# Kernel tuning notes

Measured on AMD Instinct MI355X. Metric: run time of the kernel, lower is better.

## Reference

```python
import jax, jax.numpy as jnp
import numpy as np

N, E, D, G, OUT = 100000, 1600000, 64, 2048, 16
BN_EPS = 1e-5


def setup_inputs() -> dict:
    key = jax.random.key(0)
    ks = jax.random.split(key, 24)
    s = 1.0 / np.sqrt(D)
    inp = {
        "x": jax.random.normal(ks[0], (N, D), jnp.float32),
        "edge_index": jax.random.randint(ks[1], (2, E), 0, N, jnp.int64),
        "batch": jnp.sort(jax.random.randint(ks[2], (N,), 0, G, jnp.int64)),
        # layer 0: custom_mp (mean-aggregated linear message)
        "W0": jax.random.normal(ks[3], (D, D), jnp.float32) * s,
        "b0": jnp.zeros((D,), jnp.float32),
        # layer 1: SAGE (lin_l on mean-agg neighbors + lin_r on root, lin_r bias-free)
        "Wl": jax.random.normal(ks[4], (D, D), jnp.float32) * s,
        "bl": jnp.zeros((D,), jnp.float32),
        "Wr": jax.random.normal(ks[5], (D, D), jnp.float32) * s,
        # layer 2: GIN (mlp((1+eps)*x + sum-agg), eps=0)
        "W2a": jax.random.normal(ks[6], (D, D), jnp.float32) * s,
        "b2a": jnp.zeros((D,), jnp.float32),
        "W2b": jax.random.normal(ks[7], (D, D), jnp.float32) * s,
        "b2b": jnp.zeros((D,), jnp.float32),
        # layer 3: GraphConv (lin_rel on sum-agg + bias, lin_root bias-free)
        "Wrel": jax.random.normal(ks[8], (D, D), jnp.float32) * s,
        "brel": jnp.zeros((D,), jnp.float32),
        "Wroot": jax.random.normal(ks[9], (D, D), jnp.float32) * s,
        # BatchNorm affine params per layer [4, D]
        "gammas": jnp.ones((4, D), jnp.float32),
        "betas": jnp.zeros((4, D), jnp.float32),
        # output head
        "Wout": jax.random.normal(ks[10], (D, OUT), jnp.float32) * s,
        "bout": jnp.zeros((OUT,), jnp.float32),
    }
    return inp


def _seg_sum(msgs, idx, n):
    return jax.ops.segment_sum(msgs, idx, num_segments=n)


def _mean_agg(h, src, dst, n):
    # mean of incoming messages; isolated nodes get 0 (PyG mean semantics)
    s = _seg_sum(h[src], dst, n)
    cnt = _seg_sum(jnp.ones((src.shape[0], 1), h.dtype), dst, n)
    return s / jnp.maximum(cnt, 1.0), (cnt > 0).astype(h.dtype)


def _bn_elu(h, gamma, beta):
    # training-mode BatchNorm1d (biased var) + ELU; dropout is eval-mode no-op
    mu = jnp.mean(h, axis=0)
    var = jnp.mean(jnp.square(h - mu), axis=0)
    h = (h - mu) * jax.lax.rsqrt(var + BN_EPS) * gamma + beta
    return jax.nn.elu(h)


def reference(x, edge_index, batch, W0, b0, Wl, bl, Wr, W2a, b2a, W2b, b2b,
              Wrel, brel, Wroot, gammas, betas, Wout, bout):
    src, dst = edge_index[0], edge_index[1]
    n = x.shape[0]

    # layer 0: custom_mp -> mean_j lin(x_j); lin then mean == mean then lin,
    # except bias must vanish on isolated nodes (mean of zero messages is 0).
    agg, mask = _mean_agg(x, src, dst, n)
    h = agg @ W0 + b0 * mask
    h = _bn_elu(h, gammas[0], betas[0])

    # layer 1: SAGEConv
    agg, _ = _mean_agg(h, src, dst, n)
    h = agg @ Wl + bl + h @ Wr
    h = _bn_elu(h, gammas[1], betas[1])

    # layer 2: GINConv, eps = 0
    s = _seg_sum(h[src], dst, n)
    z = (h + s) @ W2a + b2a
    h = jax.nn.relu(z) @ W2b + b2b
    h = _bn_elu(h, gammas[2], betas[2])

    # layer 3: GraphConv (sum aggregation)
    s = _seg_sum(h[src], dst, n)
    h = s @ Wrel + brel + h @ Wroot
    h = _bn_elu(h, gammas[3], betas[3])

    # global mean pool over graphs, then linear head
    ps = _seg_sum(h, batch, G)
    pc = _seg_sum(jnp.ones((n, 1), h.dtype), batch, G)
    pooled = ps / jnp.maximum(pc, 1.0)
    return pooled @ Wout + bout
```

## Files before the change

kernel.cpp:

```cpp
#include <hip/hip_runtime.h>
#include <math.h>

#define D 64
#define NB_SCAN 256

typedef unsigned short ushort_t;
typedef __attribute__((ext_vector_type(8))) short bf16x8;
typedef __attribute__((ext_vector_type(4))) float f32x4;

__device__ __forceinline__ ushort_t f2bf(float f) {
  unsigned int u = __float_as_uint(f);
  unsigned int r = (u + 0x7fffu + ((u >> 16) & 1u)) >> 16;
  return (ushort_t)r;
}

__device__ __forceinline__ float bf2f(ushort_t b) {
  return __uint_as_float((unsigned int)b << 16);
}

__global__ void hist_kernel(const int* __restrict__ dst, int* __restrict__ hist, int E) {
  int i = blockIdx.x * blockDim.x + threadIdx.x;
  int stride = gridDim.x * blockDim.x;
  for (int e = i; e < E; e += stride) {
    int d = __builtin_nontemporal_load(dst + e);
    atomicAdd(&hist[d], 1);
  }
}

__global__ void scanA_kernel(const int* __restrict__ hist, int* __restrict__ blocksum, int N) {
  __shared__ int red[256];
  int b = blockIdx.x, t = threadIdx.x;
  int chunk = (N + NB_SCAN - 1) / NB_SCAN;
  int beg = b * chunk;
  int end = min(beg + chunk, N);
  int s = 0;
  for (int i = beg + t; i < end; i += 256) s += hist[i];
  red[t] = s;
  __syncthreads();
  for (int off = 128; off > 0; off >>= 1) {
    if (t < off) red[t] += red[t + off];
    __syncthreads();
  }
  if (t == 0) blocksum[b] = red[0];
}

__global__ void scanB_kernel(const int* __restrict__ blocksum, int* __restrict__ blockoff,
                             int* __restrict__ rowptr_last) {
  __shared__ int sm[NB_SCAN];
  int t = threadIdx.x;
  sm[t] = blocksum[t];
  __syncthreads();
  for (int off = 1; off < NB_SCAN; off <<= 1) {
    int v = (t >= off) ? sm[t - off] : 0;
    __syncthreads();
    sm[t] += v;
    __syncthreads();
  }
  blockoff[t] = (t == 0) ? 0 : sm[t - 1];
  if (t == NB_SCAN - 1) rowptr_last[0] = sm[t];
}

__global__ void scanC_kernel(const int* __restrict__ hist, const int* __restrict__ blockoff,
                             int* __restrict__ rowptr, float* __restrict__ degf, int N) {
  __shared__ int sm[256];
  int b = blockIdx.x, t = threadIdx.x;
  int chunk = (N + NB_SCAN - 1) / NB_SCAN;
  int beg = b * chunk;
  int end = min(beg + chunk, N);
  int sub = (chunk + 255) / 256;
  int mybeg = beg + t * sub;
  int myend = min(mybeg + sub, end);
  int s = 0;
  for (int i = mybeg; i < myend; ++i) s += hist[i];
  sm[t] = s;
  __syncthreads();
  for (int off = 1; off < 256; off <<= 1) {
    int v = (t >= off) ? sm[t - off] : 0;
    __syncthreads();
    sm[t] += v;
    __syncthreads();
  }
  int run = blockoff[b] + ((t == 0) ? 0 : sm[t - 1]);
  for (int i = mybeg; i < myend; ++i) {
    int h = hist[i];
    rowptr[i] = run;
    degf[i] = (float)h;
    run += h;
  }
}

__global__ void fillp_kernel(const int* __restrict__ src, const int* __restrict__ dst,
                             const int* __restrict__ rowptr, int* __restrict__ cursor,
                             int* __restrict__ csr_src, int E, int N) {
  int r = blockIdx.x & 7;
  int c = blockIdx.x >> 3;
  int nchunk = gridDim.x >> 3;
  int lo = (r * N) >> 3;
  int hi = ((r + 1) * N) >> 3;
  int per = (E + nchunk - 1) / nchunk;
  int beg = c * per;
  int end = min(beg + per, E);
  for (int e = beg + (int)threadIdx.x; e < end; e += (int)blockDim.x) {
    int d = __builtin_nontemporal_load(dst + e);
    if (d >= lo && d < hi) {
      int s = __builtin_nontemporal_load(src + e);
      int pos = atomicAdd(&cursor[d], 1);
      csr_src[rowptr[d] + pos] = s;
    }
  }
}

__global__ void cvt_kernel(const float* __restrict__ in, ushort_t* __restrict__ outb, int total4) {
  int i = blockIdx.x * blockDim.x + threadIdx.x;
  int stride = gridDim.x * blockDim.x;
  const float4* in4 = (const float4*)in;
  for (int idx = i; idx < total4; idx += stride) {
    float4 v = in4[idx];
    ushort4 u;
    u.x = f2bf(v.x); u.y = f2bf(v.y); u.z = f2bf(v.z); u.w = f2bf(v.w);
    ((ushort4*)outb)[idx] = u;
  }
}

__global__ void packw_kernel(const float* __restrict__ W, ushort_t* __restrict__ Wp) {
  int idx = blockIdx.x * blockDim.x + threadIdx.x;
  if (idx >= 4096) return;
  int i = idx & 7;
  int lane = (idx >> 3) & 63;
  int ct = (idx >> 9) & 3;
  int kt = idx >> 11;
  int k = kt * 32 + ((lane >> 4) << 3) + i;
  int c = (ct << 4) + (lane & 15);
  Wp[idx] = f2bf(W[k * D + c]);
}

__global__ void gatherb_kernel(const ushort_t* __restrict__ hb, const int* __restrict__ rowptr,
                               const int* __restrict__ csr_src, ushort_t* __restrict__ aggb, int N) {
  int lane = threadIdx.x & 63;
  int wid = (blockIdx.x * blockDim.x + threadIdx.x) >> 6;
  int nw = (gridDim.x * blockDim.x) >> 6;
  int e4 = lane >> 4;
  int c4 = lane & 15;
  for (int n = wid; n < N; n += nw) {
    int beg = __builtin_amdgcn_readfirstlane(rowptr[n]);
    int end = __builtin_amdgcn_readfirstlane(rowptr[n + 1]);
    float ax = 0.f, ay = 0.f, az = 0.f, aw = 0.f;
    float bx = 0.f, by = 0.f, bz = 0.f, bw = 0.f;
    for (int k = beg; k < end; k += 64) {
      int myidx = (k + lane < end) ? csr_src[k + lane] : 0;
      int cnt = end - k; if (cnt > 64) cnt = 64;
      int i = 0;
      for (; i + 7 < cnt; i += 8) {
        int ia = __shfl(myidx, i + e4);
        int ib = __shfl(myidx, i + 4 + e4);
        uint2 pa = *(const uint2*)(hb + (size_t)ia * D + (c4 << 2));
        uint2 pb = *(const uint2*)(hb + (size_t)ib * D + (c4 << 2));
        ax += __uint_as_float(pa.x << 16);
        ay += __uint_as_float(pa.x & 0xffff0000u);
        az += __uint_as_float(pa.y << 16);
        aw += __uint_as_float(pa.y & 0xffff0000u);
        bx += __uint_as_float(pb.x << 16);
        by += __uint_as_float(pb.x & 0xffff0000u);
        bz += __uint_as_float(pb.y << 16);
        bw += __uint_as_float(pb.y & 0xffff0000u);
      }
      for (; i < cnt; i += 4) {
        int is = i + e4;
        int ia = __shfl(myidx, is & 63);
        if (is < cnt) {
          uint2 pa = *(const uint2*)(hb + (size_t)ia * D + (c4 << 2));
          ax += __uint_as_float(pa.x << 16);
          ay += __uint_as_float(pa.x & 0xffff0000u);
          az += __uint_as_float(pa.y << 16);
          aw += __uint_as_float(pa.y & 0xffff0000u);
        }
      }
    }
    float sx = ax + bx, sy = ay + by, sz = az + bz, sw = aw + bw;
    sx += __shfl_xor(sx, 16); sx += __shfl_xor(sx, 32);
    sy += __shfl_xor(sy, 16); sy += __shfl_xor(sy, 32);
    sz += __shfl_xor(sz, 16); sz += __shfl_xor(sz, 32);
    sw += __shfl_xor(sw, 16); sw += __shfl_xor(sw, 32);
    if (lane < 16) {
      ushort4 u;
      u.x = f2bf(sx); u.y = f2bf(sy); u.z = f2bf(sz); u.w = f2bf(sw);
      *(ushort4*)(aggb + (size_t)n * D + (c4 << 2)) = u;
    }
  }
}

template <int DUAL, int SCALEA, int MASKB, int RELU, int STATS, int OUTBF>
__global__ __launch_bounds__(256, 4)
void mmx_kernel(const ushort_t* __restrict__ A1, const ushort_t* __restrict__ A2,
                const ushort_t* __restrict__ Wp1, const ushort_t* __restrict__ Wp2,
                const float* __restrict__ bias, const float* __restrict__ deg,
                float* __restrict__ outf, ushort_t* __restrict__ outb,
                float* __restrict__ stats, int N) {
  int lane = threadIdx.x & 63;
  int wv = (blockIdx.x * blockDim.x + threadIdx.x) >> 6;
  int nw = (gridDim.x * blockDim.x) >> 6;
  int T = (N + 15) >> 4;
  int lr = lane & 15;
  int lk = lane >> 4;
  float s1[4] = {0.f, 0.f, 0.f, 0.f};
  float s2[4] = {0.f, 0.f, 0.f, 0.f};

  for (int t = wv; t < T; t += nw) {
    int r0 = t << 4;
    int rowA = r0 + lr;
    if (rowA >= N) rowA = N - 1;
    const ushort_t* pa = A1 + (size_t)rowA * D + (lk << 3);
    bf16x8 a1k0 = *(const bf16x8*)(pa);
    bf16x8 a1k1 = *(const bf16x8*)(pa + 32);
    bf16x8 a2k0{}, a2k1{};
    if constexpr (DUAL) {
      const ushort_t* ph = A2 + (size_t)rowA * D + (lk << 3);
      a2k0 = *(const bf16x8*)(ph);
      a2k1 = *(const bf16x8*)(ph + 32);
    }
    float invd[4], msk[4];
#pragma unroll
    for (int rg = 0; rg < 4; ++rg) {
      if constexpr (SCALEA || MASKB) {
        int rr = r0 + (lk << 2) + rg;
        if (rr >= N) rr = N - 1;
        float dv = deg[rr];
        invd[rg] = 1.0f / fmaxf(dv, 1.0f);
        msk[rg] = (dv > 0.f) ? 1.f : 0.f;
      } else {
        invd[rg] = 1.f; msk[rg] = 1.f;
      }
    }

#pragma unroll
    for (int ct = 0; ct < 4; ++ct) {
      bf16x8 w1k0 = *(const bf16x8*)(Wp1 + (((0 * 4 + ct) * 64 + lane) << 3));
      bf16x8 w1k1 = *(const bf16x8*)(Wp1 + (((1 * 4 + ct) * 64 + lane) << 3));
      f32x4 accA = {0.f, 0.f, 0.f, 0.f};
      accA = __builtin_amdgcn_mfma_f32_16x16x32_bf16(a1k0, w1k0, accA, 0, 0, 0);
      accA = __builtin_amdgcn_mfma_f32_16x16x32_bf16(a1k1, w1k1, accA, 0, 0, 0);
      f32x4 accH = {0.f, 0.f, 0.f, 0.f};
      if constexpr (DUAL) {
        bf16x8 w2k0 = *(const bf16x8*)(Wp2 + (((0 * 4 + ct) * 64 + lane) << 3));
        bf16x8 w2k1 = *(const bf16x8*)(Wp2 + (((1 * 4 + ct) * 64 + lane) << 3));
        accH = __builtin_amdgcn_mfma_f32_16x16x32_bf16(a2k0, w2k0, accH, 0, 0, 0);
        accH = __builtin_amdgcn_mfma_f32_16x16x32_bf16(a2k1, w2k1, accH, 0, 0, 0);
      }
      float bj = bias[(ct << 4) + lr];
#pragma unroll
      for (int rg = 0; rg < 4; ++rg) {
        int row = r0 + (lk << 2) + rg;
        float v = accA[rg];
        if constexpr (SCALEA) v *= invd[rg];
        if constexpr (DUAL) v += accH[rg];
        if constexpr (MASKB) v += bj * msk[rg]; else v += bj;
        if constexpr (RELU) v = fmaxf(v, 0.f);
        if (row < N) {
          int col = (ct << 4) + lr;
          if constexpr (OUTBF) outb[(size_t)row * D + col] = f2bf(v);
          else outf[(size_t)row * D + col] = v;
          if constexpr (STATS) { s1[ct] += v; s2[ct] += v * v; }
        }
      }
    }
  }

  if constexpr (STATS) {
    __shared__ float red[2][4][256];
#pragma unroll
    for (int ct = 0; ct < 4; ++ct) {
      red[0][ct][threadIdx.x] = s1[ct];
      red[1][ct][threadIdx.x] = s2[ct];
    }
    __syncthreads();
    int tt = threadIdx.x;
    if (tt < 64) {
      int ct = tt >> 4, base = tt & 15;
      float t1 = 0.f, t2 = 0.f;
      for (int i = 0; i < 16; ++i) {
        t1 += red[0][ct][base + i * 16];
        t2 += red[1][ct][base + i * 16];
      }
      atomicAdd(&stats[tt], t1);
      atomicAdd(&stats[D + tt], t2);
    }
  }
}

__global__ void bn_coef_kernel(const float* __restrict__ stats, const float* __restrict__ gamma,
                               const float* __restrict__ beta, float* __restrict__ coef,
                               float invN) {
  int j = threadIdx.x;
  if (j < D) {
    float mu = stats[j] * invN;
    float var = fmaxf(stats[D + j] * invN - mu * mu, 0.f);
    float rs = rsqrtf(var + 1e-5f);
    float sc = gamma[j] * rs;
    coef[j] = sc;
    coef[D + j] = beta[j] - mu * sc;
  }
}

__global__ void apply_kernel(const ushort_t* __restrict__ hpre, const float* __restrict__ coef,
                             ushort_t* __restrict__ hb, int total4) {
  int i = blockIdx.x * blockDim.x + threadIdx.x;
  int stride = gridDim.x * blockDim.x;
  const ushort4* in4 = (const ushort4*)hpre;
  const float4* c4 = (const float4*)coef;
  for (int idx = i; idx < total4; idx += stride) {
    int col4 = idx & 15;
    float4 sc = c4[col4];
    float4 sh = c4[16 + col4];
    ushort4 vu = in4[idx];
    float4 r;
    r.x = bf2f(vu.x) * sc.x + sh.x;
    r.y = bf2f(vu.y) * sc.y + sh.y;
    r.z = bf2f(vu.z) * sc.z + sh.z;
    r.w = bf2f(vu.w) * sc.w + sh.w;
    r.x = r.x > 0.f ? r.x : __expf(r.x) - 1.f;
    r.y = r.y > 0.f ? r.y : __expf(r.y) - 1.f;
    r.z = r.z > 0.f ? r.z : __expf(r.z) - 1.f;
    r.w = r.w > 0.f ? r.w : __expf(r.w) - 1.f;
    ushort4 u;
    u.x = f2bf(r.x); u.y = f2bf(r.y); u.z = f2bf(r.z); u.w = f2bf(r.w);
    ((ushort4*)hb)[idx] = u;
  }
}

__global__ void pool_kernel(const ushort_t* __restrict__ hb, const int* __restrict__ batch,
                            float* __restrict__ pooled, float* __restrict__ pcnt, int N) {
  int lane = threadIdx.x & 63;
  int wid = (blockIdx.x * blockDim.x + threadIdx.x) >> 6;
  int nw = (gridDim.x * blockDim.x) >> 6;
  for (int n = wid; n < N; n += nw) {
    int b = batch[n];
    unsigned int u = (unsigned int)hb[(size_t)n * D + lane] << 16;
    atomicAdd(&pooled[(size_t)b * D + lane], __uint_as_float(u));
    if (lane == 0) atomicAdd(&pcnt[b], 1.0f);
  }
}

__global__ void head_kernel(const float* __restrict__ pooled, const float* __restrict__ pcnt,
                            const float* __restrict__ Wout, const float* __restrict__ bout,
                            float* __restrict__ outp, int G) {
  int idx = blockIdx.x * blockDim.x + threadIdx.x;
  if (idx >= G * 16) return;
  int g = idx >> 4;
  int o = idx & 15;
  float inv = 1.0f / fmaxf(pcnt[g], 1.0f);
  float acc = 0.f;
#pragma unroll
  for (int i = 0; i < D; ++i) acc += pooled[(size_t)g * D + i] * Wout[i * 16 + o];
  outp[idx] = acc * inv + bout[o];
}

extern "C" void kernel_launch(void* const* d_in, const int* in_sizes, int n_in,
                              void* d_out, int out_size, void* d_ws, size_t ws_size,
                              hipStream_t stream) {
  (void)n_in; (void)ws_size;
  const float* x      = (const float*)d_in[0];
  const int*   edge   = (const int*)d_in[1];
  const int*   batch  = (const int*)d_in[2];
  const float* W0     = (const float*)d_in[3];
  const float* b0     = (const float*)d_in[4];
  const float* Wl     = (const float*)d_in[5];
  const float* bl     = (const float*)d_in[6];
  const float* Wr     = (const float*)d_in[7];
  const float* W2a    = (const float*)d_in[8];
  const float* b2a    = (const float*)d_in[9];
  const float* W2b    = (const float*)d_in[10];
  const float* b2b    = (const float*)d_in[11];
  const float* Wrel   = (const float*)d_in[12];
  const float* brel   = (const float*)d_in[13];
  const float* Wroot  = (const float*)d_in[14];
  const float* gammas = (const float*)d_in[15];
  const float* betas  = (const float*)d_in[16];
  const float* Wout   = (const float*)d_in[17];
  const float* bout   = (const float*)d_in[18];
  float* out = (float*)d_out;

  int N = in_sizes[0] / D;
  int E = in_sizes[1] / 2;
  int G = out_size / 16;
  const int* src = edge;
  const int* dst = edge + E;

  float* ws = (float*)d_ws;
  float* deg  = ws;
  float* stats = deg + N;
  float* coef  = stats + 2 * D;
  float* pooled = coef + 2 * D;
  float* pcnt   = pooled + (size_t)G * D;
  int* hist    = (int*)(pcnt + G);
  int* rowptr  = hist + N;
  int* csr_src = rowptr + N + 1;
  int* blocksum = csr_src + E;
  int* blockoff = blocksum + NB_SCAN;
  ushort_t* hb   = (ushort_t*)(blockoff + NB_SCAN);
  ushort_t* aggb = hb + (size_t)N * D;
  ushort_t* zb   = aggb + (size_t)N * D;
  ushort_t* hpb  = zb + (size_t)N * D;
  ushort_t* wp0   = hpb + (size_t)N * D;
  ushort_t* wpl   = wp0 + 4096;
  ushort_t* wpr   = wpl + 4096;
  ushort_t* wp2a  = wpr + 4096;
  ushort_t* wp2b  = wp2a + 4096;
  ushort_t* wprel = wp2b + 4096;
  ushort_t* wproot = wprel + 4096;

  int total4 = N * D / 4;
  int gather_blocks = (N * 64 + 255) / 256;
  if (gather_blocks > 8192) gather_blocks = 8192;
  int mmx_blocks = 1024;

  hipMemsetAsync(hist, 0, N * sizeof(int), stream);
  hist_kernel<<<1024, 256, 0, stream>>>(dst, hist, E);
  scanA_kernel<<<NB_SCAN, 256, 0, stream>>>(hist, blocksum, N);
  scanB_kernel<<<1, NB_SCAN, 0, stream>>>(blocksum, blockoff, rowptr + N);
  scanC_kernel<<<NB_SCAN, 256, 0, stream>>>(hist, blockoff, rowptr, deg, N);
  hipMemsetAsync(hist, 0, N * sizeof(int), stream);
  fillp_kernel<<<1024, 256, 0, stream>>>(src, dst, rowptr, hist, csr_src, E, N);

  packw_kernel<<<16, 256, 0, stream>>>(W0, wp0);
  packw_kernel<<<16, 256, 0, stream>>>(Wl, wpl);
  packw_kernel<<<16, 256, 0, stream>>>(Wr, wpr);
  packw_kernel<<<16, 256, 0, stream>>>(W2a, wp2a);
  packw_kernel<<<16, 256, 0, stream>>>(W2b, wp2b);
  packw_kernel<<<16, 256, 0, stream>>>(Wrel, wprel);
  packw_kernel<<<16, 256, 0, stream>>>(Wroot, wproot);

  cvt_kernel<<<2048, 256, 0, stream>>>(x, hb, total4);
  gatherb_kernel<<<gather_blocks, 256, 0, stream>>>(hb, rowptr, csr_src, aggb, N);
  hipMemsetAsync(stats, 0, 2 * D * sizeof(float), stream);
  mmx_kernel<0, 1, 1, 0, 1, 1><<<mmx_blocks, 256, 0, stream>>>(
      aggb, nullptr, wp0, nullptr, b0, deg, nullptr, hpb, stats, N);
  bn_coef_kernel<<<1, 64, 0, stream>>>(stats, gammas + 0 * D, betas + 0 * D, coef, 1.0f / N);
  apply_kernel<<<2048, 256, 0, stream>>>(hpb, coef, hb, total4);

  gatherb_kernel<<<gather_blocks, 256, 0, stream>>>(hb, rowptr, csr_src, aggb, N);
  hipMemsetAsync(stats, 0, 2 * D * sizeof(float), stream);
  mmx_kernel<1, 1, 0, 0, 1, 1><<<mmx_blocks, 256, 0, stream>>>(
      aggb, hb, wpl, wpr, bl, deg, nullptr, hpb, stats, N);
  bn_coef_kernel<<<1, 64, 0, stream>>>(stats, gammas + 1 * D, betas + 1 * D, coef, 1.0f / N);
  apply_kernel<<<2048, 256, 0, stream>>>(hpb, coef, hb, total4);

  gatherb_kernel<<<gather_blocks, 256, 0, stream>>>(hb, rowptr, csr_src, aggb, N);
  mmx_kernel<1, 0, 0, 1, 0, 1><<<mmx_blocks, 256, 0, stream>>>(
      aggb, hb, wp2a, wp2a, b2a, deg, nullptr, zb, nullptr, N);
  hipMemsetAsync(stats, 0, 2 * D * sizeof(float), stream);
  mmx_kernel<0, 0, 0, 0, 1, 1><<<mmx_blocks, 256, 0, stream>>>(
      zb, nullptr, wp2b, nullptr, b2b, deg, nullptr, hpb, stats, N);
  bn_coef_kernel<<<1, 64, 0, stream>>>(stats, gammas + 2 * D, betas + 2 * D, coef, 1.0f / N);
  apply_kernel<<<2048, 256, 0, stream>>>(hpb, coef, hb, total4);

  gatherb_kernel<<<gather_blocks, 256, 0, stream>>>(hb, rowptr, csr_src, aggb, N);
  hipMemsetAsync(stats, 0, 2 * D * sizeof(float), stream);
  mmx_kernel<1, 0, 0, 0, 1, 1><<<mmx_blocks, 256, 0, stream>>>(
      aggb, hb, wprel, wproot, brel, deg, nullptr, hpb, stats, N);
  bn_coef_kernel<<<1, 64, 0, stream>>>(stats, gammas + 3 * D, betas + 3 * D, coef, 1.0f / N);
  apply_kernel<<<2048, 256, 0, stream>>>(hpb, coef, hb, total4);

  hipMemsetAsync(pooled, 0, (size_t)G * D * sizeof(float), stream);
  hipMemsetAsync(pcnt, 0, G * sizeof(float), stream);
  pool_kernel<<<1024, 256, 0, stream>>>(hb, batch, pooled, pcnt, N);
  head_kernel<<<(G * 16 + 255) / 256, 256, 0, stream>>>(pooled, pcnt, Wout, bout, out, G);
}
```

Baseline: 638.4 us.

## Fuse BN coefficients into apply, fuse final BN-ELU into pooling, unroll short-row gather

Each apply kernel now computes its BatchNorm scale and shift in shared memory from the stats, so the separate bn_coef launches go away. The four per-layer memsets become one up-front memset over four stats slices. The last layer's BN+ELU is folded into the pooling kernel, which removes one full apply pass over N×64 activations. The gather kernel gains a fully unrolled path for rows with at most 64 edges, with predicated loads, so more loads can be in flight, at the cost of some wasted loads on padding slots.

```diff
diff --git a/kernel.cpp b/kernel.cpp
--- a/kernel.cpp
+++ b/kernel.cpp
@@ -134,6 +134,13 @@
   Wp[idx] = f2bf(W[k * D + c]);
 }
 
+#define GSTEP(j) { int i0 = 4 * (j) + e4; \
+  int ia = __shfl(myidx, i0 & 63); \
+  uint2 p = *(const uint2*)(hb + (size_t)ia * D + (c4 << 2)); \
+  if (i0 >= cnt) { p.x = 0u; p.y = 0u; } \
+  ax += __uint_as_float(p.x << 16); ay += __uint_as_float(p.x & 0xffff0000u); \
+  az += __uint_as_float(p.y << 16); aw += __uint_as_float(p.y & 0xffff0000u); }
+
 __global__ void gatherb_kernel(const ushort_t* __restrict__ hb, const int* __restrict__ rowptr,
                                const int* __restrict__ csr_src, ushort_t* __restrict__ aggb, int N) {
   int lane = threadIdx.x & 63;
@@ -144,46 +151,60 @@
   for (int n = wid; n < N; n += nw) {
     int beg = __builtin_amdgcn_readfirstlane(rowptr[n]);
     int end = __builtin_amdgcn_readfirstlane(rowptr[n + 1]);
+    int cnt = end - beg;
     float ax = 0.f, ay = 0.f, az = 0.f, aw = 0.f;
-    float bx = 0.f, by = 0.f, bz = 0.f, bw = 0.f;
-    for (int k = beg; k < end; k += 64) {
-      int myidx = (k + lane < end) ? csr_src[k + lane] : 0;
-      int cnt = end - k; if (cnt > 64) cnt = 64;
-      int i = 0;
-      for (; i + 7 < cnt; i += 8) {
-        int ia = __shfl(myidx, i + e4);
-        int ib = __shfl(myidx, i + 4 + e4);
-        uint2 pa = *(const uint2*)(hb + (size_t)ia * D + (c4 << 2));
-        uint2 pb = *(const uint2*)(hb + (size_t)ib * D + (c4 << 2));
-        ax += __uint_as_float(pa.x << 16);
-        ay += __uint_as_float(pa.x & 0xffff0000u);
-        az += __uint_as_float(pa.y << 16);
-        aw += __uint_as_float(pa.y & 0xffff0000u);
-        bx += __uint_as_float(pb.x << 16);
-        by += __uint_as_float(pb.x & 0xffff0000u);
-        bz += __uint_as_float(pb.y << 16);
-        bw += __uint_as_float(pb.y & 0xffff0000u);
-      }
-      for (; i < cnt; i += 4) {
-        int is = i + e4;
-        int ia = __shfl(myidx, is & 63);
-        if (is < cnt) {
+    if (cnt <= 64) {
+      int myidx = (lane < cnt) ? csr_src[beg + lane] : 0;
+      if (cnt <= 16) {
+        GSTEP(0) GSTEP(1) GSTEP(2) GSTEP(3)
+      } else if (cnt <= 32) {
+        GSTEP(0) GSTEP(1) GSTEP(2) GSTEP(3)
+        GSTEP(4) GSTEP(5) GSTEP(6) GSTEP(7)
+      } else {
+        GSTEP(0) GSTEP(1) GSTEP(2) GSTEP(3)
+        GSTEP(4) GSTEP(5) GSTEP(6) GSTEP(7)
+        GSTEP(8) GSTEP(9) GSTEP(10) GSTEP(11)
+        GSTEP(12) GSTEP(13) GSTEP(14) GSTEP(15)
+      }
+    } else {
+      for (int k = beg; k < end; k += 64) {
+        int myidx = (k + lane < end) ? csr_src[k + lane] : 0;
+        int cc = end - k; if (cc > 64) cc = 64;
+        int i = 0;
+        for (; i + 7 < cc; i += 8) {
+          int ia = __shfl(myidx, i + e4);
+          int ib = __shfl(myidx, i + 4 + e4);
           uint2 pa = *(const uint2*)(hb + (size_t)ia * D + (c4 << 2));
+          uint2 pb = *(const uint2*)(hb + (size_t)ib * D + (c4 << 2));
           ax += __uint_as_float(pa.x << 16);
           ay += __uint_as_float(pa.x & 0xffff0000u);
           az += __uint_as_float(pa.y << 16);
           aw += __uint_as_float(pa.y & 0xffff0000u);
+          ax += __uint_as_float(pb.x << 16);
+          ay += __uint_as_float(pb.x & 0xffff0000u);
+          az += __uint_as_float(pb.y << 16);
+          aw += __uint_as_float(pb.y & 0xffff0000u);
         }
-      }
-    }
-    float sx = ax + bx, sy = ay + by, sz = az + bz, sw = aw + bw;
-    sx += __shfl_xor(sx, 16); sx += __shfl_xor(sx, 32);
-    sy += __shfl_xor(sy, 16); sy += __shfl_xor(sy, 32);
-    sz += __shfl_xor(sz, 16); sz += __shfl_xor(sz, 32);
-    sw += __shfl_xor(sw, 16); sw += __shfl_xor(sw, 32);
+        for (; i < cc; i += 4) {
+          int is = i + e4;
+          int ia = __shfl(myidx, is & 63);
+          if (is < cc) {
+            uint2 pa = *(const uint2*)(hb + (size_t)ia * D + (c4 << 2));
+            ax += __uint_as_float(pa.x << 16);
+            ay += __uint_as_float(pa.x & 0xffff0000u);
+            az += __uint_as_float(pa.y << 16);
+            aw += __uint_as_float(pa.y & 0xffff0000u);
+          }
+        }
+      }
+    }
+    ax += __shfl_xor(ax, 16); ax += __shfl_xor(ax, 32);
+    ay += __shfl_xor(ay, 16); ay += __shfl_xor(ay, 32);
+    az += __shfl_xor(az, 16); az += __shfl_xor(az, 32);
+    aw += __shfl_xor(aw, 16); aw += __shfl_xor(aw, 32);
     if (lane < 16) {
       ushort4 u;
-      u.x = f2bf(sx); u.y = f2bf(sy); u.z = f2bf(sz); u.w = f2bf(sw);
+      u.x = f2bf(ax); u.y = f2bf(ay); u.z = f2bf(az); u.w = f2bf(aw);
       *(ushort4*)(aggb + (size_t)n * D + (c4 << 2)) = u;
     }
   }
@@ -287,30 +308,27 @@
   }
 }
 
-__global__ void bn_coef_kernel(const float* __restrict__ stats, const float* __restrict__ gamma,
-                               const float* __restrict__ beta, float* __restrict__ coef,
-                               float invN) {
-  int j = threadIdx.x;
-  if (j < D) {
-    float mu = stats[j] * invN;
-    float var = fmaxf(stats[D + j] * invN - mu * mu, 0.f);
+__global__ void apply_kernel(const ushort_t* __restrict__ hpre, const float* __restrict__ stats,
+                             const float* __restrict__ gamma, const float* __restrict__ beta,
+                             float invN, ushort_t* __restrict__ hb, int total4) {
+  __shared__ float cf[128];
+  int t = threadIdx.x;
+  if (t < 64) {
+    float mu = stats[t] * invN;
+    float var = fmaxf(stats[D + t] * invN - mu * mu, 0.f);
     float rs = rsqrtf(var + 1e-5f);
-    float sc = gamma[j] * rs;
-    coef[j] = sc;
-    coef[D + j] = beta[j] - mu * sc;
-  }
-}
-
-__global__ void apply_kernel(const ushort_t* __restrict__ hpre, const float* __restrict__ coef,
-                             ushort_t* __restrict__ hb, int total4) {
-  int i = blockIdx.x * blockDim.x + threadIdx.x;
+    float sc = gamma[t] * rs;
+    cf[t] = sc;
+    cf[64 + t] = beta[t] - mu * sc;
+  }
+  __syncthreads();
+  int i = blockIdx.x * blockDim.x + t;
   int stride = gridDim.x * blockDim.x;
   const ushort4* in4 = (const ushort4*)hpre;
-  const float4* c4 = (const float4*)coef;
   for (int idx = i; idx < total4; idx += stride) {
     int col4 = idx & 15;
-    float4 sc = c4[col4];
-    float4 sh = c4[16 + col4];
+    float4 sc = *(const float4*)(cf + col4 * 4);
+    float4 sh = *(const float4*)(cf + 64 + col4 * 4);
     ushort4 vu = in4[idx];
     float4 r;
     r.x = bf2f(vu.x) * sc.x + sh.x;
@@ -327,15 +345,30 @@
   }
 }
 
-__global__ void pool_kernel(const ushort_t* __restrict__ hb, const int* __restrict__ batch,
-                            float* __restrict__ pooled, float* __restrict__ pcnt, int N) {
-  int lane = threadIdx.x & 63;
-  int wid = (blockIdx.x * blockDim.x + threadIdx.x) >> 6;
+__global__ void poolapply_kernel(const ushort_t* __restrict__ hpre, const float* __restrict__ stats,
+                                 const float* __restrict__ gamma, const float* __restrict__ beta,
+                                 float invN, const int* __restrict__ batch,
+                                 float* __restrict__ pooled, float* __restrict__ pcnt, int N) {
+  __shared__ float cf[128];
+  int t = threadIdx.x;
+  if (t < 64) {
+    float mu = stats[t] * invN;
+    float var = fmaxf(stats[D + t] * invN - mu * mu, 0.f);
+    float rs = rsqrtf(var + 1e-5f);
+    float sc = gamma[t] * rs;
+    cf[t] = sc;
+    cf[64 + t] = beta[t] - mu * sc;
+  }
+  __syncthreads();
+  int lane = t & 63;
+  int wid = (blockIdx.x * blockDim.x + t) >> 6;
   int nw = (gridDim.x * blockDim.x) >> 6;
+  float sc = cf[lane], sh = cf[64 + lane];
   for (int n = wid; n < N; n += nw) {
     int b = batch[n];
-    unsigned int u = (unsigned int)hb[(size_t)n * D + lane] << 16;
-    atomicAdd(&pooled[(size_t)b * D + lane], __uint_as_float(u));
+    float v = bf2f(hpre[(size_t)n * D + lane]) * sc + sh;
+    v = v > 0.f ? v : __expf(v) - 1.f;
+    atomicAdd(&pooled[(size_t)b * D + lane], v);
     if (lane == 0) atomicAdd(&pcnt[b], 1.0f);
   }
 }
@@ -388,8 +421,7 @@
   float* ws = (float*)d_ws;
   float* deg  = ws;
   float* stats = deg + N;
-  float* coef  = stats + 2 * D;
-  float* pooled = coef + 2 * D;
+  float* pooled = stats + 4 * 2 * D;
   float* pcnt   = pooled + (size_t)G * D;
   int* hist    = (int*)(pcnt + G);
   int* rowptr  = hist + N;
@@ -412,8 +444,10 @@
   int gather_blocks = (N * 64 + 255) / 256;
   if (gather_blocks > 8192) gather_blocks = 8192;
   int mmx_blocks = 1024;
+  float invN = 1.0f / (float)N;
 
   hipMemsetAsync(hist, 0, N * sizeof(int), stream);
+  hipMemsetAsync(stats, 0, 4 * 2 * D * sizeof(float), stream);
   hist_kernel<<<1024, 256, 0, stream>>>(dst, hist, E);
   scanA_kernel<<<NB_SCAN, 256, 0, stream>>>(hist, blocksum, N);
   scanB_kernel<<<1, NB_SCAN, 0, stream>>>(blocksum, blockoff, rowptr + N);
@@ -431,37 +465,29 @@
 
   cvt_kernel<<<2048, 256, 0, stream>>>(x, hb, total4);
   gatherb_kernel<<<gather_blocks, 256, 0, stream>>>(hb, rowptr, csr_src, aggb, N);
-  hipMemsetAsync(stats, 0, 2 * D * sizeof(float), stream);
   mmx_kernel<0, 1, 1, 0, 1, 1><<<mmx_blocks, 256, 0, stream>>>(
-      aggb, nullptr, wp0, nullptr, b0, deg, nullptr, hpb, stats, N);
-  bn_coef_kernel<<<1, 64, 0, stream>>>(stats, gammas + 0 * D, betas + 0 * D, coef, 1.0f / N);
-  apply_kernel<<<2048, 256, 0, stream>>>(hpb, coef, hb, total4);
+      aggb, nullptr, wp0, nullptr, b0, deg, nullptr, hpb, stats + 0 * 128, N);
+  apply_kernel<<<2048, 256, 0, stream>>>(hpb, stats + 0 * 128, gammas + 0 * D, betas + 0 * D, invN, hb, total4);
 
   gatherb_kernel<<<gather_blocks, 256, 0, stream>>>(hb, rowptr, csr_src, aggb, N);
-  hipMemsetAsync(stats, 0, 2 * D * sizeof(float), stream);
   mmx_kernel<1, 1, 0, 0, 1, 1><<<mmx_blocks, 256, 0, stream>>>(
-      aggb, hb, wpl, wpr, bl, deg, nullptr, hpb, stats, N);
-  bn_coef_kernel<<<1, 64, 0, stream>>>(stats, gammas + 1 * D, betas + 1 * D, coef, 1.0f / N);
-  apply_kernel<<<2048, 256, 0, stream>>>(hpb, coef, hb, total4);
+      aggb, hb, wpl, wpr, bl, deg, nullptr, hpb, stats + 1 * 128, N);
+  apply_kernel<<<2048, 256, 0, stream>>>(hpb, stats + 1 * 128, gammas + 1 * D, betas + 1 * D, invN, hb, total4);
 
   gatherb_kernel<<<gather_blocks, 256, 0, stream>>>(hb, rowptr, csr_src, aggb, N);
   mmx_kernel<1, 0, 0, 1, 0, 1><<<mmx_blocks, 256, 0, stream>>>(
       aggb, hb, wp2a, wp2a, b2a, deg, nullptr, zb, nullptr, N);
-  hipMemsetAsync(stats, 0, 2 * D * sizeof(float), stream);
   mmx_kernel<0, 0, 0, 0, 1, 1><<<mmx_blocks, 256, 0, stream>>>(
-      zb, nullptr, wp2b, nullptr, b2b, deg, nullptr, hpb, stats, N);
-  bn_coef_kernel<<<1, 64, 0, stream>>>(stats, gammas + 2 * D, betas + 2 * D, coef, 1.0f / N);
-  apply_kernel<<<2048, 256, 0, stream>>>(hpb, coef, hb, total4);
+      zb, nullptr, wp2b, nullptr, b2b, deg, nullptr, hpb, stats + 2 * 128, N);
+  apply_kernel<<<2048, 256, 0, stream>>>(hpb, stats + 2 * 128, gammas + 2 * D, betas + 2 * D, invN, hb, total4);
 
   gatherb_kernel<<<gather_blocks, 256, 0, stream>>>(hb, rowptr, csr_src, aggb, N);
-  hipMemsetAsync(stats, 0, 2 * D * sizeof(float), stream);
   mmx_kernel<1, 0, 0, 0, 1, 1><<<mmx_blocks, 256, 0, stream>>>(
-      aggb, hb, wprel, wproot, brel, deg, nullptr, hpb, stats, N);
-  bn_coef_kernel<<<1, 64, 0, stream>>>(stats, gammas + 3 * D, betas + 3 * D, coef, 1.0f / N);
-  apply_kernel<<<2048, 256, 0, stream>>>(hpb, coef, hb, total4);
+      aggb, hb, wprel, wproot, brel, deg, nullptr, hpb, stats + 3 * 128, N);
 
   hipMemsetAsync(pooled, 0, (size_t)G * D * sizeof(float), stream);
   hipMemsetAsync(pcnt, 0, G * sizeof(float), stream);
-  pool_kernel<<<1024, 256, 0, stream>>>(hb, batch, pooled, pcnt, N);
+  poolapply_kernel<<<1024, 256, 0, stream>>>(hpb, stats + 3 * 128, gammas + 3 * D, betas + 3 * D,
+                                             invN, batch, pooled, pcnt, N);
   head_kernel<<<(G * 16 + 255) / 256, 256, 0, stream>>>(pooled, pcnt, Wout, bout, out, G);
 }
```

Measured after the change: 618.1 us. 3.2% less time.
